# Optimization experiments

Measured on AMD Instinct MI355X. Metric: run time of the kernel, lower is better.

Reference implementation:

```python
import jax, jax.numpy as jnp
import numpy as np

TAU = 0.01  # softmax temperature used throughout the module


def _cross_en(sim_matrix):
    # -mean(diag(log_softmax(sim, -1)))
    logpt = jax.nn.log_softmax(sim_matrix, axis=-1)
    return -jnp.mean(jnp.diagonal(logpt))


def setup_inputs() -> dict:
    key = jax.random.key(0)
    k1, k2, k3, k4 = jax.random.split(key, 4)
    bs, nw, nf, d = 128, 80, 64, 768
    inp = {
        "traj_output": jax.random.normal(k1, (bs, d), dtype=jnp.float32),
        "frame_features": jax.random.normal(k2, (bs, nf, d), dtype=jnp.float32),
        "sentence_output": jax.random.normal(k3, (bs, d), dtype=jnp.float32),
        "word_features": jax.random.normal(k4, (bs, nw, d), dtype=jnp.float32),
        # nn.Parameter(torch.eye(...)) -- init_weights does not touch these
        "global_mat_weight": jnp.eye(d, dtype=jnp.float32),
        "word_logit_weight": jnp.eye(nw, dtype=jnp.float32),
        "frame_logit_weight": jnp.eye(nf, dtype=jnp.float32),
        "local_mat_weight": jnp.eye(d, dtype=jnp.float32),
        "frame_mat_weight": jnp.eye(nf, dtype=jnp.float32),
        "word_mat_weight": jnp.eye(nw, dtype=jnp.float32),
        "frame_mat_weight2": jnp.eye(nf, dtype=jnp.float32),
        "word_mat_weight2": jnp.eye(nw, dtype=jnp.float32),
    }
    return inp


def reference(traj_output, frame_features, sentence_output, word_features,
              global_mat_weight, word_logit_weight, frame_logit_weight,
              local_mat_weight, frame_mat_weight, word_mat_weight,
              frame_mat_weight2, word_mat_weight2):
    # traj_output: [bs,d]; frame_features: [bs,nf,d]; sentence_output: [bs,d]; word_features: [bs,nw,d]

    # --- traj_sent: (sent @ G) @ traj^T -> [bs_t, bs_v] ---
    traj_sent_sim = (sentence_output @ global_mat_weight) @ traj_output.T

    # --- video_word: word_features @ traj^T -> [bs_t, nw, bs_v] ---
    A = jnp.einsum('twd,vd->twv', word_features, traj_output)
    sA = jax.nn.softmax(A / TAU, axis=1)
    # (softmax.permute(0,2,1) @ W).permute(0,2,1): contract nw axis with W
    wA = jnp.einsum('twv,wu->tuv', sA, word_logit_weight)
    video_word_sim = jnp.sum(A * wA, axis=1)  # [bs_t, bs_v]

    # --- sentence_frame: sent x frame -> [bs_v, bs_t, nf] (torch broadcast batching) ---
    B = jnp.einsum('td,vfd->vtf', sentence_output, frame_features)
    sB = jax.nn.softmax(B / TAU, axis=-1)
    sentence_frame_sim = jnp.sum(B * (sB @ frame_logit_weight), axis=-1).T  # [bs_t, bs_v]

    # --- frame_word: fine-grained sim [bs_t, nw, bs_v, nf] ---
    S = jnp.einsum('twd,vfd->twvf', word_features @ local_mat_weight, frame_features)
    # word-level logit: softmax over nw, mix with word_mat_weight, weighted sum over nw
    sw = jax.nn.softmax(S / TAU, axis=1)
    word_level = jnp.sum(jnp.einsum('twvf,wu->tuvf', sw, word_mat_weight) * S, axis=1)  # [t,v,f]
    # frame-level logit: softmax over nf, mix with frame_mat_weight, weighted sum over nf
    sf = jax.nn.softmax(S / TAU, axis=-1)
    frame_level = jnp.sum((sf @ frame_mat_weight) * S, axis=-1)  # [t,w,v]
    # sent2frame: reduce nf of word_level
    smw = jax.nn.softmax(word_level / TAU, axis=-1)
    sent2frame = jnp.sum((smw @ frame_mat_weight2) * word_level, axis=-1)  # [t,v]
    # video2word: reduce nw of frame_level
    smf = jax.nn.softmax(frame_level / TAU, axis=1)
    video2word = jnp.sum(jnp.einsum('twv,wu->tuv', smf, word_mat_weight2) * frame_level, axis=1)  # [t,v]
    frame_word_sim = (sent2frame + video2word) / 2.0

    sim_matrix = (traj_sent_sim + video_word_sim + sentence_frame_sim + frame_word_sim) / 4.0

    sim_loss = (_cross_en(sim_matrix) + _cross_en(sim_matrix.T)) / 2.0
    return sim_loss
```

## Files before the change

kernel.cpp:

```cpp
#include <hip/hip_runtime.h>
#include <math.h>

#define BS 128
#define NW 80
#define NF 64
#define DD 768
#define INV_TAU 100.0f

typedef unsigned short u16;
typedef unsigned int u32;
typedef __attribute__((ext_vector_type(8))) short bf16x8;
typedef __attribute__((ext_vector_type(4))) float f32x4;

__device__ __forceinline__ u16 f2bf(float x) {
    unsigned b = __float_as_uint(x);
    return (u16)((b + 0x7fffu + ((b >> 16) & 1u)) >> 16);
}
__device__ __forceinline__ float bf2f(u16 h) { return __uint_as_float(((unsigned)h) << 16); }

__device__ __forceinline__ void gload_lds16(const void* gsrc, void* ldst) {
    __builtin_amdgcn_global_load_lds(
        (const __attribute__((address_space(1))) unsigned int*)gsrc,
        (__attribute__((address_space(3))) unsigned int*)ldst, 16, 0, 0);
}

__global__ __launch_bounds__(256) void k_sent_global(
    const float* __restrict__ sent, const float* __restrict__ G, float* __restrict__ sg)
{
    int idx = blockIdx.x * 256 + threadIdx.x;
    int t = idx / DD, e = idx % DD;
    const float* srow = sent + t * DD;
    float acc = 0.f;
    #pragma unroll 4
    for (int d = 0; d < DD; ++d) acc += srow[d] * G[d * DD + e];
    sg[idx] = acc;
}

__global__ __launch_bounds__(256) void k_traj_sent(
    const float* __restrict__ sg, const float* __restrict__ traj, float* __restrict__ sim)
{
    __shared__ float ss[16][33], tt[16][33];
    int tx = threadIdx.x & 15, ty = threadIdx.x >> 4;
    int t0 = blockIdx.y * 16, v0 = blockIdx.x * 16;
    float acc = 0.f;
    for (int kk = 0; kk < DD; kk += 32) {
        for (int l = threadIdx.x; l < 16 * 32; l += 256) {
            int r = l >> 5, c = l & 31;
            ss[r][c] = sg[(t0 + r) * DD + kk + c];
            tt[r][c] = traj[(v0 + r) * DD + kk + c];
        }
        __syncthreads();
        #pragma unroll
        for (int k = 0; k < 32; ++k) acc += ss[ty][k] * tt[tx][k];
        __syncthreads();
    }
    sim[(t0 + ty) * BS + v0 + tx] = 0.25f * acc;
}

__global__ __launch_bounds__(256) void k_prepw(
    const float* __restrict__ Wm, const float* __restrict__ Fm,
    u16* __restrict__ WmT_hi, u16* __restrict__ WmT_lo,
    u16* __restrict__ FmT_hi, u16* __restrict__ FmT_lo)
{
    int gid = blockIdx.x * 256 + threadIdx.x;
    if (gid < 80 * 96) {
        int u = gid / 96, w = gid % 96;
        float x = (w < 80) ? Wm[w * 80 + u] : 0.f;
        u16 h = f2bf(x);
        WmT_hi[gid] = h; WmT_lo[gid] = f2bf(x - bf2f(h));
    } else if (gid < 80 * 96 + 64 * 64) {
        int j = gid - 80 * 96;
        int fp = j >> 6, f = j & 63;
        float x = Fm[f * 64 + fp];
        u16 h = f2bf(x);
        FmT_hi[j] = h; FmT_lo[j] = f2bf(x - bf2f(h));
    }
}

__global__ __launch_bounds__(256) void k_ffsplit(
    const float* __restrict__ x, u16* __restrict__ hi, u16* __restrict__ lo)
{
    int i = blockIdx.x * 256 + threadIdx.x;
    float4 f = *(const float4*)&x[(size_t)i * 4];
    ushort4 h, l;
    h.x = f2bf(f.x); l.x = f2bf(f.x - bf2f(h.x));
    h.y = f2bf(f.y); l.y = f2bf(f.y - bf2f(h.y));
    h.z = f2bf(f.z); l.z = f2bf(f.z - bf2f(h.z));
    h.w = f2bf(f.w); l.w = f2bf(f.w - bf2f(h.w));
    *(ushort4*)&hi[(size_t)i * 4] = h;
    *(ushort4*)&lo[(size_t)i * 4] = l;
}

__global__ __launch_bounds__(256, 2) void k_wl(
    const float* __restrict__ wf, const float* __restrict__ L,
    u16* __restrict__ wl_hi, u16* __restrict__ wl_lo)
{
    __shared__ u16 Ah[128][72], Al[128][72];
    __shared__ u16 Bh[128][72], Bl[128][72];
    const int tid = threadIdx.x;
    const int lane = tid & 63, wid = tid >> 6;
    const int m0 = blockIdx.y * 128, n0 = blockIdx.x * 128;

    f32x4 acc[2][8];
    #pragma unroll
    for (int i = 0; i < 2; ++i)
        #pragma unroll
        for (int j = 0; j < 8; ++j) acc[i][j] = (f32x4){0.f, 0.f, 0.f, 0.f};

    for (int kk = 0; kk < DD; kk += 64) {
        #pragma unroll
        for (int p = 0; p < 8; ++p) {
            int row = p * 16 + (tid >> 4), c4 = tid & 15;
            float4 v = *(const float4*)&wf[(size_t)(m0 + row) * DD + kk + c4 * 4];
            ushort4 h, l;
            h.x = f2bf(v.x); l.x = f2bf(v.x - bf2f(h.x));
            h.y = f2bf(v.y); l.y = f2bf(v.y - bf2f(h.y));
            h.z = f2bf(v.z); l.z = f2bf(v.z - bf2f(h.z));
            h.w = f2bf(v.w); l.w = f2bf(v.w - bf2f(h.w));
            *(ushort4*)&Ah[row][c4 * 4] = h;
            *(ushort4*)&Al[row][c4 * 4] = l;
        }
        #pragma unroll
        for (int p = 0; p < 8; ++p) {
            int kr = p * 8 + (tid >> 5), c4 = tid & 31;
            float4 v = *(const float4*)&L[(size_t)(kk + kr) * DD + n0 + c4 * 4];
            #pragma unroll
            for (int jj = 0; jj < 4; ++jj) {
                int n = c4 * 4 + jj;
                float x = (jj == 0) ? v.x : (jj == 1) ? v.y : (jj == 2) ? v.z : v.w;
                u16 h = f2bf(x);
                int ka = kr ^ ((n & 7) << 3);
                Bh[n][ka] = h;
                Bl[n][ka] = f2bf(x - bf2f(h));
            }
        }
        __syncthreads();
        #pragma unroll
        for (int ks = 0; ks < 2; ++ks) {
            int koff = ks * 32 + (lane >> 4) * 8;
            bf16x8 ah[2], al[2];
            #pragma unroll
            for (int i = 0; i < 2; ++i) {
                int row = wid * 32 + 16 * i + (lane & 15);
                ah[i] = *(const bf16x8*)&Ah[row][koff];
                al[i] = *(const bf16x8*)&Al[row][koff];
            }
            #pragma unroll
            for (int j = 0; j < 8; ++j) {
                int n = 16 * j + (lane & 15);
                int kb = koff ^ ((n & 7) << 3);
                bf16x8 bh = *(const bf16x8*)&Bh[n][kb];
                bf16x8 bl = *(const bf16x8*)&Bl[n][kb];
                #pragma unroll
                for (int i = 0; i < 2; ++i) {
                    acc[i][j] = __builtin_amdgcn_mfma_f32_16x16x32_bf16(ah[i], bh, acc[i][j], 0, 0, 0);
                    acc[i][j] = __builtin_amdgcn_mfma_f32_16x16x32_bf16(ah[i], bl, acc[i][j], 0, 0, 0);
                    acc[i][j] = __builtin_amdgcn_mfma_f32_16x16x32_bf16(al[i], bh, acc[i][j], 0, 0, 0);
                }
            }
        }
        __syncthreads();
    }
    #pragma unroll
    for (int i = 0; i < 2; ++i)
        #pragma unroll
        for (int j = 0; j < 8; ++j)
            #pragma unroll
            for (int r = 0; r < 4; ++r) {
                float x = acc[i][j][r];
                int row = m0 + wid * 32 + 16 * i + ((lane >> 4) << 2) + r;
                int col = n0 + 16 * j + (lane & 15);
                size_t idx = (size_t)row * DD + col;
                u16 h = f2bf(x);
                wl_hi[idx] = h;
                wl_lo[idx] = f2bf(x - bf2f(h));
            }
}

__global__ __launch_bounds__(256, 2) void k_video_word(
    const float* __restrict__ wf, const float* __restrict__ traj,
    const float* __restrict__ Wl, float* __restrict__ sim)
{
    __shared__ __align__(16) float As[NW][36];
    __shared__ __align__(16) float Bs[64][36];
    __shared__ float Am[NW][65];
    __shared__ float Pm[NW][65];
    int tx = threadIdx.x & 15, ty = threadIdx.x >> 4;
    int t = blockIdx.y, v0 = blockIdx.x * 64;
    const float* wft = wf + t * NW * DD;
    float acc[5][4] = {};
    for (int kk = 0; kk < DD; kk += 32) {
        for (int l = threadIdx.x; l < NW * 32; l += 256) {
            int w = l >> 5, k = l & 31;
            As[w][k] = wft[w * DD + kk + k];
        }
        for (int l = threadIdx.x; l < 64 * 32; l += 256) {
            int v = l >> 5, k = l & 31;
            Bs[v][k] = traj[(v0 + v) * DD + kk + k];
        }
        __syncthreads();
        #pragma unroll
        for (int k = 0; k < 32; k += 4) {
            float4 a[5], b[4];
            #pragma unroll
            for (int i = 0; i < 5; ++i) a[i] = *(const float4*)&As[tx + 16 * i][k];
            #pragma unroll
            for (int j = 0; j < 4; ++j) b[j] = *(const float4*)&Bs[ty + 16 * j][k];
            #pragma unroll
            for (int i = 0; i < 5; ++i)
                #pragma unroll
                for (int j = 0; j < 4; ++j)
                    acc[i][j] += a[i].x * b[j].x + a[i].y * b[j].y + a[i].z * b[j].z + a[i].w * b[j].w;
        }
        __syncthreads();
    }
    #pragma unroll
    for (int i = 0; i < 5; ++i)
        #pragma unroll
        for (int j = 0; j < 4; ++j) Am[tx + 16 * i][ty + 16 * j] = acc[i][j];
    __syncthreads();
    if (threadIdx.x < 64) {
        int v = threadIdx.x;
        float m = -1e30f;
        for (int w = 0; w < NW; ++w) m = fmaxf(m, Am[w][v]);
        float s = 0.f;
        for (int w = 0; w < NW; ++w) { float e = __expf((Am[w][v] - m) * INV_TAU); Pm[w][v] = e; s += e; }
        float r = 1.f / s;
        for (int w = 0; w < NW; ++w) Pm[w][v] *= r;
    }
    __syncthreads();
    float mm[5][4] = {};
    for (int w = 0; w < NW; ++w) {
        float a[5], b[4];
        #pragma unroll
        for (int i = 0; i < 5; ++i) a[i] = Wl[w * NW + tx + 16 * i];
        #pragma unroll
        for (int j = 0; j < 4; ++j) b[j] = Pm[w][ty + 16 * j];
        #pragma unroll
        for (int i = 0; i < 5; ++i)
            #pragma unroll
            for (int j = 0; j < 4; ++j) mm[i][j] += a[i] * b[j];
    }
    #pragma unroll
    for (int j = 0; j < 4; ++j) {
        float p = 0.f;
        #pragma unroll
        for (int i = 0; i < 5; ++i) p += mm[i][j] * Am[tx + 16 * i][ty + 16 * j];
        for (int o = 8; o; o >>= 1) p += __shfl_xor(p, o, 16);
        if (tx == 0) sim[t * BS + v0 + ty + 16 * j] += 0.25f * p;
    }
}

__global__ __launch_bounds__(256, 2) void k_sent_frame(
    const float* __restrict__ sent, const float* __restrict__ ff,
    const float* __restrict__ Fl, float* __restrict__ sim)
{
    __shared__ __align__(16) float Ss[64][36];
    __shared__ __align__(16) float Fs[64][36];
    __shared__ float Bm[64][65];
    __shared__ float Pm[64][65];
    int tx = threadIdx.x & 15, ty = threadIdx.x >> 4;
    int v = blockIdx.y, t0 = blockIdx.x * 64;
    const float* ffv = ff + v * NF * DD;
    float acc[4][4] = {};
    for (int kk = 0; kk < DD; kk += 32) {
        for (int l = threadIdx.x; l < 64 * 32; l += 256) {
            int r = l >> 5, k = l & 31;
            Ss[r][k] = sent[(t0 + r) * DD + kk + k];
            Fs[r][k] = ffv[r * DD + kk + k];
        }
        __syncthreads();
        #pragma unroll
        for (int k = 0; k < 32; k += 4) {
            float4 a[4], b[4];
            #pragma unroll
            for (int i = 0; i < 4; ++i) a[i] = *(const float4*)&Ss[tx + 16 * i][k];
            #pragma unroll
            for (int j = 0; j < 4; ++j) b[j] = *(const float4*)&Fs[ty + 16 * j][k];
            #pragma unroll
            for (int i = 0; i < 4; ++i)
                #pragma unroll
                for (int j = 0; j < 4; ++j)
                    acc[i][j] += a[i].x * b[j].x + a[i].y * b[j].y + a[i].z * b[j].z + a[i].w * b[j].w;
        }
        __syncthreads();
    }
    #pragma unroll
    for (int i = 0; i < 4; ++i)
        #pragma unroll
        for (int j = 0; j < 4; ++j) Bm[tx + 16 * i][ty + 16 * j] = acc[i][j];
    __syncthreads();
    if (threadIdx.x < 64) {
        int r = threadIdx.x;
        float m = -1e30f;
        for (int f = 0; f < NF; ++f) m = fmaxf(m, Bm[r][f]);
        float s = 0.f;
        for (int f = 0; f < NF; ++f) { float e = __expf((Bm[r][f] - m) * INV_TAU); Pm[r][f] = e; s += e; }
        float rr = 1.f / s;
        for (int f = 0; f < NF; ++f) Pm[r][f] *= rr;
    }
    __syncthreads();
    float nn[4][4] = {};
    for (int f = 0; f < NF; ++f) {
        float a[4], b[4];
        #pragma unroll
        for (int i = 0; i < 4; ++i) a[i] = Pm[ty + 16 * i][f];
        #pragma unroll
        for (int j = 0; j < 4; ++j) b[j] = Fl[f * NF + tx + 16 * j];
        #pragma unroll
        for (int i = 0; i < 4; ++i)
            #pragma unroll
            for (int j = 0; j < 4; ++j) nn[i][j] += a[i] * b[j];
    }
    #pragma unroll
    for (int i = 0; i < 4; ++i) {
        float p = 0.f;
        #pragma unroll
        for (int j = 0; j < 4; ++j) p += nn[i][j] * Bm[ty + 16 * i][tx + 16 * j];
        for (int o = 8; o; o >>= 1) p += __shfl_xor(p, o, 16);
        if (tx == 0) sim[(t0 + ty + 16 * i) * BS + v] += 0.25f * p;
    }
}

__global__ __launch_bounds__(256, 4) void k_frame_word(
    const u16* __restrict__ wl_hi, const u16* __restrict__ wl_lo,
    const u16* __restrict__ ff_hi, const u16* __restrict__ ff_lo,
    const u16* __restrict__ WmT_hi, const u16* __restrict__ WmT_lo,
    const u16* __restrict__ FmT_hi, const u16* __restrict__ FmT_lo,
    const float* __restrict__ F2, const float* __restrict__ Wm2,
    float* __restrict__ sim)
{
    __shared__ __align__(16) union SH {
        u16 stage[18432];
        struct Post {
            float Sm[80][65];
            float redm[4][64], reds[4][64];
            float colM[64], colRD[64];
            float rowM[80], rowRD[80];
            float wlv[64], flv[80], flvp[4][80];
            float smw[64], smf[80];
            float s2f, v2w;
        } post;
    } sh;

    const int tid = threadIdx.x;
    const int lane = tid & 63, wid = tid >> 6;
    const int col = lane & 15, grp = lane >> 4;
    const int v = blockIdx.x, t = blockIdx.y;

    f32x4 acc[5], acc2[5];
    #pragma unroll
    for (int i = 0; i < 5; ++i) { acc[i] = (f32x4){0.f,0.f,0.f,0.f}; acc2[i] = (f32x4){0.f,0.f,0.f,0.f}; }

    const int r8 = lane >> 3, s8 = lane & 7;
    const int gk = s8 ^ r8;

    for (int kk = 0; kk < DD; kk += 64) {
        for (int seg = wid; seg < 36; seg += 4) {
            const u16* src;
            int ldsoff;
            if (seg < 10) {
                int g = seg, row = g * 8 + r8;
                src = wl_hi + (size_t)(t * NW + row) * DD + kk + gk * 8;
                ldsoff = g * 512;
            } else if (seg < 20) {
                int g = seg - 10, row = g * 8 + r8;
                src = wl_lo + (size_t)(t * NW + row) * DD + kk + gk * 8;
                ldsoff = 5120 + g * 512;
            } else if (seg < 28) {
                int g = seg - 20, row = g * 8 + r8;
                src = ff_hi + (size_t)(v * NF + row) * DD + kk + gk * 8;
                ldsoff = 10240 + g * 512;
            } else {
                int g = seg - 28, row = g * 8 + r8;
                src = ff_lo + (size_t)(v * NF + row) * DD + kk + gk * 8;
                ldsoff = 14336 + g * 512;
            }
            gload_lds16(src, (void*)&sh.stage[ldsoff]);
        }
        __syncthreads();
        const u16* st = sh.stage;
        #pragma unroll
        for (int ks = 0; ks < 2; ++ks) {
            const int sl = (ks << 2) + grp;
            bf16x8 afh[5], afl[5], bfh, bfl;
            #pragma unroll
            for (int i = 0; i < 5; ++i) {
                int row = col + 16 * i;
                int off = row * 64 + ((sl ^ (row & 7)) << 3);
                afh[i] = *(const bf16x8*)&st[off];
                afl[i] = *(const bf16x8*)&st[5120 + off];
            }
            {
                int row = col + 16 * wid;
                int off = row * 64 + ((sl ^ (row & 7)) << 3);
                bfh = *(const bf16x8*)&st[10240 + off];
                bfl = *(const bf16x8*)&st[14336 + off];
            }
            #pragma unroll
            for (int i = 0; i < 5; ++i)
                acc[i] = __builtin_amdgcn_mfma_f32_16x16x32_bf16(afh[i], bfh, acc[i], 0, 0, 0);
            #pragma unroll
            for (int i = 0; i < 5; ++i)
                acc2[i] = __builtin_amdgcn_mfma_f32_16x16x32_bf16(afh[i], bfl, acc2[i], 0, 0, 0);
            #pragma unroll
            for (int i = 0; i < 5; ++i)
                acc[i] = __builtin_amdgcn_mfma_f32_16x16x32_bf16(afl[i], bfh, acc[i], 0, 0, 0);
        }
        __syncthreads();
    }

    #pragma unroll
    for (int i = 0; i < 5; ++i)
        #pragma unroll
        for (int r = 0; r < 4; ++r)
            sh.post.Sm[16 * i + (grp << 2) + r][col + (wid << 4)] = acc[i][r] + acc2[i][r];
    __syncthreads();

    {
        const int f = tid & 63, q = tid >> 6, w0 = q * 20;
        float m = -1e30f;
        for (int w = w0; w < w0 + 20; ++w) m = fmaxf(m, sh.post.Sm[w][f]);
        float s = 0.f;
        for (int w = w0; w < w0 + 20; ++w) s += __expf((sh.post.Sm[w][f] - m) * INV_TAU);
        sh.post.redm[q][f] = m; sh.post.reds[q][f] = s;
        __syncthreads();
        if (q == 0) {
            float M = -1e30f;
            #pragma unroll
            for (int qq = 0; qq < 4; ++qq) M = fmaxf(M, sh.post.redm[qq][f]);
            float Dn = 0.f;
            #pragma unroll
            for (int qq = 0; qq < 4; ++qq) Dn += sh.post.reds[qq][f] * __expf((sh.post.redm[qq][f] - M) * INV_TAU);
            sh.post.colM[f] = M;
            sh.post.colRD[f] = 1.f / Dn;
        }
    }
    __syncthreads();

    {
        f32x4 d1[5], d1b[5];
        #pragma unroll
        for (int i = 0; i < 5; ++i) { d1[i] = (f32x4){0.f,0.f,0.f,0.f}; d1b[i] = (f32x4){0.f,0.f,0.f,0.f}; }
        const int f = wid * 16 + col;
        const float Mf = sh.post.colM[f], RDf = sh.post.colRD[f];
        #pragma unroll
        for (int ks = 0; ks < 3; ++ks) {
            const int w0 = ks * 32 + grp * 8;
            union { u16 h[8]; bf16x8 v; } bh, bl;
            #pragma unroll
            for (int j = 0; j < 8; ++j) {
                int w = w0 + j;
                int wc = (w < NW) ? w : 0;
                float e = __expf((sh.post.Sm[wc][f] - Mf) * INV_TAU) * RDf;
                e = (w < NW) ? e : 0.f;
                u16 hh = f2bf(e);
                bh.h[j] = hh;
                bl.h[j] = f2bf(e - bf2f(hh));
            }
            #pragma unroll
            for (int i = 0; i < 5; ++i) {
                int aaddr = (16 * i + col) * 96 + ks * 32 + grp * 8;
                bf16x8 ah = *(const bf16x8*)&WmT_hi[aaddr];
                bf16x8 al = *(const bf16x8*)&WmT_lo[aaddr];
                d1[i]  = __builtin_amdgcn_mfma_f32_16x16x32_bf16(ah, bh.v, d1[i], 0, 0, 0);
                d1b[i] = __builtin_amdgcn_mfma_f32_16x16x32_bf16(ah, bl.v, d1b[i], 0, 0, 0);
                d1[i]  = __builtin_amdgcn_mfma_f32_16x16x32_bf16(al, bh.v, d1[i], 0, 0, 0);
            }
        }
        float p = 0.f;
        #pragma unroll
        for (int i = 0; i < 5; ++i)
            #pragma unroll
            for (int r = 0; r < 4; ++r)
                p += (d1[i][r] + d1b[i][r]) * sh.post.Sm[16 * i + (grp << 2) + r][f];
        p += __shfl_xor(p, 16);
        p += __shfl_xor(p, 32);
        if (lane < 16) sh.post.wlv[wid * 16 + lane] = p;
    }
    __syncthreads();

    if (tid < 160) {
        const int w = tid >> 1, h = tid & 1, f0 = h * 32;
        float m = -1e30f;
        for (int c = 0; c < 32; ++c) m = fmaxf(m, sh.post.Sm[w][f0 + c]);
        m = fmaxf(m, __shfl_xor(m, 1));
        float s = 0.f;
        for (int c = 0; c < 32; ++c) s += __expf((sh.post.Sm[w][f0 + c] - m) * INV_TAU);
        s += __shfl_xor(s, 1);
        if (h == 0) { sh.post.rowM[w] = m; sh.post.rowRD[w] = 1.f / s; }
    }
    __syncthreads();

    {
        f32x4 d2[5], d2b[5];
        #pragma unroll
        for (int i = 0; i < 5; ++i) { d2[i] = (f32x4){0.f,0.f,0.f,0.f}; d2b[i] = (f32x4){0.f,0.f,0.f,0.f}; }
        #pragma unroll
        for (int ks = 0; ks < 2; ++ks) {
            int baddr = (wid * 16 + col) * 64 + ks * 32 + grp * 8;
            bf16x8 bh = *(const bf16x8*)&FmT_hi[baddr];
            bf16x8 bl = *(const bf16x8*)&FmT_lo[baddr];
            #pragma unroll
            for (int i = 0; i < 5; ++i) {
                const int row = 16 * i + col;
                const float Mw = sh.post.rowM[row], RDw = sh.post.rowRD[row];
                const int f0 = ks * 32 + grp * 8;
                union { u16 h[8]; bf16x8 v; } ah, al;
                #pragma unroll
                for (int j = 0; j < 8; ++j) {
                    float e = __expf((sh.post.Sm[row][f0 + j] - Mw) * INV_TAU) * RDw;
                    u16 hh = f2bf(e);
                    ah.h[j] = hh;
                    al.h[j] = f2bf(e - bf2f(hh));
                }
                d2[i]  = __builtin_amdgcn_mfma_f32_16x16x32_bf16(ah.v, bh, d2[i], 0, 0, 0);
                d2b[i] = __builtin_amdgcn_mfma_f32_16x16x32_bf16(ah.v, bl, d2b[i], 0, 0, 0);
                d2[i]  = __builtin_amdgcn_mfma_f32_16x16x32_bf16(al.v, bh, d2[i], 0, 0, 0);
            }
        }
        #pragma unroll
        for (int i = 0; i < 5; ++i)
            #pragma unroll
            for (int r = 0; r < 4; ++r) {
                int w = 16 * i + (grp << 2) + r;
                float p = (d2[i][r] + d2b[i][r]) * sh.post.Sm[w][wid * 16 + col];
                p += __shfl_xor(p, 1);
                p += __shfl_xor(p, 2);
                p += __shfl_xor(p, 4);
                p += __shfl_xor(p, 8);
                if (col == 0) sh.post.flvp[wid][w] = p;
            }
    }
    __syncthreads();
    if (tid < 80)
        sh.post.flv[tid] = sh.post.flvp[0][tid] + sh.post.flvp[1][tid]
                         + sh.post.flvp[2][tid] + sh.post.flvp[3][tid];
    __syncthreads();

    if (wid == 0) {
        float x = sh.post.wlv[lane];
        float m = x;
        #pragma unroll
        for (int o = 32; o; o >>= 1) m = fmaxf(m, __shfl_xor(m, o));
        float e = __expf((x - m) * INV_TAU);
        float s = e;
        #pragma unroll
        for (int o = 32; o; o >>= 1) s += __shfl_xor(s, o);
        sh.post.smw[lane] = e / s;
    } else if (wid == 1) {
        float x0 = sh.post.flv[lane];
        float x1 = (lane < 16) ? sh.post.flv[64 + lane] : -1e30f;
        float m = fmaxf(x0, x1);
        #pragma unroll
        for (int o = 32; o; o >>= 1) m = fmaxf(m, __shfl_xor(m, o));
        float e0 = __expf((x0 - m) * INV_TAU);
        float e1 = (lane < 16) ? __expf((x1 - m) * INV_TAU) : 0.f;
        float s = e0 + e1;
        #pragma unroll
        for (int o = 32; o; o >>= 1) s += __shfl_xor(s, o);
        sh.post.smf[lane] = e0 / s;
        if (lane < 16) sh.post.smf[64 + lane] = e1 / s;
    }
    __syncthreads();

    if (wid == 0) {
        float g = 0.f;
        for (int f = 0; f < NF; ++f) g += sh.post.smw[f] * F2[f * NF + lane];
        float p = g * sh.post.wlv[lane];
        #pragma unroll
        for (int o = 32; o; o >>= 1) p += __shfl_xor(p, o);
        if (lane == 0) sh.post.s2f = p;
    } else if (wid == 1) {
        float g = 0.f;
        for (int w = 0; w < NW; ++w) g += sh.post.smf[w] * Wm2[w * NW + lane];
        float p = g * sh.post.flv[lane];
        if (lane < 16) {
            float g2 = 0.f;
            for (int w = 0; w < NW; ++w) g2 += sh.post.smf[w] * Wm2[w * NW + 64 + lane];
            p += g2 * sh.post.flv[64 + lane];
        }
        #pragma unroll
        for (int o = 32; o; o >>= 1) p += __shfl_xor(p, o);
        if (lane == 0) sh.post.v2w = p;
    }
    __syncthreads();
    if (tid == 0) sim[t * BS + v] += 0.125f * (sh.post.s2f + sh.post.v2w);
}

__global__ __launch_bounds__(256) void k_loss(const float* __restrict__ sim, float* __restrict__ out)
{
    __shared__ float S[BS][BS + 1];
    __shared__ float lr[BS], lc[BS];
    for (int l = threadIdx.x; l < BS * BS; l += 256) {
        int r = l >> 7, c = l & 127;
        S[r][c] = sim[l];
    }
    __syncthreads();
    int tid = threadIdx.x;
    if (tid < BS) {
        float m = -1e30f;
        for (int c = 0; c < BS; ++c) m = fmaxf(m, S[tid][c]);
        float s = 0.f;
        for (int c = 0; c < BS; ++c) s += __expf(S[tid][c] - m);
        lr[tid] = m + __logf(s);
    } else {
        int c = tid - BS;
        float m = -1e30f;
        for (int r = 0; r < BS; ++r) m = fmaxf(m, S[r][c]);
        float s = 0.f;
        for (int r = 0; r < BS; ++r) s += __expf(S[r][c] - m);
        lc[c] = m + __logf(s);
    }
    __syncthreads();
    if (tid == 0) {
        float a = 0.f;
        for (int i = 0; i < BS; ++i) a += S[i][i] - 0.5f * lr[i] - 0.5f * lc[i];
        out[0] = -a / (float)BS;
    }
}

extern "C" void kernel_launch(void* const* d_in, const int* in_sizes, int n_in,
                              void* d_out, int out_size, void* d_ws, size_t ws_size,
                              hipStream_t stream)
{
    const float* traj = (const float*)d_in[0];
    const float* ff   = (const float*)d_in[1];
    const float* sent = (const float*)d_in[2];
    const float* wf   = (const float*)d_in[3];
    const float* G    = (const float*)d_in[4];
    const float* Wl   = (const float*)d_in[5];
    const float* Fl   = (const float*)d_in[6];
    const float* L    = (const float*)d_in[7];
    const float* Fm   = (const float*)d_in[8];
    const float* Wm   = (const float*)d_in[9];
    const float* F2   = (const float*)d_in[10];
    const float* Wm2  = (const float*)d_in[11];
    float* out = (float*)d_out;
    char* base = (char*)d_ws;

    float* sg     = (float*)(base);
    float* sim    = (float*)(base + 393216);
    u16*   wl_hi  = (u16*)(base + 458752);
    u16*   wl_lo  = (u16*)(base + 16187392);
    u16*   ff_hi  = (u16*)(base + 31916032);
    u16*   ff_lo  = (u16*)(base + 44498944);
    u16*   WmT_hi = (u16*)(base + 57081856);
    u16*   WmT_lo = (u16*)(base + 57097216);
    u16*   FmT_hi = (u16*)(base + 57112576);
    u16*   FmT_lo = (u16*)(base + 57120768);

    hipLaunchKernelGGL(k_sent_global, dim3(BS * DD / 256), dim3(256), 0, stream, sent, G, sg);
    hipLaunchKernelGGL(k_traj_sent, dim3(8, 8), dim3(256), 0, stream, sg, traj, sim);
    hipLaunchKernelGGL(k_prepw, dim3(46), dim3(256), 0, stream, Wm, Fm, WmT_hi, WmT_lo, FmT_hi, FmT_lo);
    hipLaunchKernelGGL(k_ffsplit, dim3(BS * NF * DD / 1024), dim3(256), 0, stream, ff, ff_hi, ff_lo);
    hipLaunchKernelGGL(k_wl, dim3(6, 80), dim3(256), 0, stream, wf, L, wl_hi, wl_lo);
    hipLaunchKernelGGL(k_video_word, dim3(2, BS), dim3(256), 0, stream, wf, traj, Wl, sim);
    hipLaunchKernelGGL(k_sent_frame, dim3(2, BS), dim3(256), 0, stream, sent, ff, Fl, sim);
    hipLaunchKernelGGL(k_frame_word, dim3(BS, BS), dim3(256), 0, stream,
                       wl_hi, wl_lo, ff_hi, ff_lo, WmT_hi, WmT_lo, FmT_hi, FmT_lo, F2, Wm2, sim);
    hipLaunchKernelGGL(k_loss, dim3(1), dim3(256), 0, stream, sim, out);
}
```

Measured before the change: 1.483 ms.

## Restructure frame-word epilogue: apply softmax after weight mixing, keep S in registers

The post-GEMM stage of k_frame_word no longer stores S as fp32 in shared memory and exponentiates it inside the MFMA operand build. It splits S once into bf16 hi/lo copies in two layouts and multiplies S by the mixing weights with MFMA. The softmax probabilities are computed in registers with shuffle reductions and applied afterwards, relying on linearity so normalisation becomes a scalar multiply. This cuts repeated exp evaluations, shared-memory traffic and some barriers. In exchange the weight prep layout changes, launch bounds drop to 3 blocks per SIMD, and the bf16 split of S changes the rounding error profile.

After: 1.905 ms. 28.4% more time.

```diff
diff --git a/kernel.cpp b/kernel.cpp
--- a/kernel.cpp
+++ b/kernel.cpp
@@ -59,21 +59,20 @@
 
 __global__ __launch_bounds__(256) void k_prepw(
     const float* __restrict__ Wm, const float* __restrict__ Fm,
-    u16* __restrict__ WmT_hi, u16* __restrict__ WmT_lo,
-    u16* __restrict__ FmT_hi, u16* __restrict__ FmT_lo)
+    u16* __restrict__ Wm_hi, u16* __restrict__ Wm_lo,
+    u16* __restrict__ Fm_hi, u16* __restrict__ Fm_lo)
 {
     int gid = blockIdx.x * 256 + threadIdx.x;
     if (gid < 80 * 96) {
-        int u = gid / 96, w = gid % 96;
-        float x = (w < 80) ? Wm[w * 80 + u] : 0.f;
+        int w = gid / 96, u = gid % 96;
+        float x = (u < 80) ? Wm[w * 80 + u] : 0.f;
         u16 h = f2bf(x);
-        WmT_hi[gid] = h; WmT_lo[gid] = f2bf(x - bf2f(h));
+        Wm_hi[gid] = h; Wm_lo[gid] = f2bf(x - bf2f(h));
     } else if (gid < 80 * 96 + 64 * 64) {
         int j = gid - 80 * 96;
-        int fp = j >> 6, f = j & 63;
-        float x = Fm[f * 64 + fp];
+        float x = Fm[j];
         u16 h = f2bf(x);
-        FmT_hi[j] = h; FmT_lo[j] = f2bf(x - bf2f(h));
+        Fm_hi[j] = h; Fm_lo[j] = f2bf(x - bf2f(h));
     }
 }
 
@@ -322,22 +321,22 @@
     }
 }
 
-__global__ __launch_bounds__(256, 4) void k_frame_word(
+__global__ __launch_bounds__(256, 3) void k_frame_word(
     const u16* __restrict__ wl_hi, const u16* __restrict__ wl_lo,
     const u16* __restrict__ ff_hi, const u16* __restrict__ ff_lo,
-    const u16* __restrict__ WmT_hi, const u16* __restrict__ WmT_lo,
-    const u16* __restrict__ FmT_hi, const u16* __restrict__ FmT_lo,
+    const u16* __restrict__ Wm_hi, const u16* __restrict__ Wm_lo,
+    const u16* __restrict__ Fm_hi, const u16* __restrict__ Fm_lo,
     const float* __restrict__ F2, const float* __restrict__ Wm2,
     float* __restrict__ sim)
 {
     __shared__ __align__(16) union SH {
         u16 stage[18432];
         struct Post {
-            float Sm[80][65];
-            float redm[4][64], reds[4][64];
-            float colM[64], colRD[64];
+            u16 Swf_h[80][72], Swf_l[80][72];
+            u16 Sfw_h[64][104], Sfw_l[64][104];
+            float part[2][4][80];
             float rowM[80], rowRD[80];
-            float wlv[64], flv[80], flvp[4][80];
+            float wlv[64], flv[80];
             float smw[64], smf[80];
             float s2f, v2w;
         } post;
@@ -347,6 +346,7 @@
     const int lane = tid & 63, wid = tid >> 6;
     const int col = lane & 15, grp = lane >> 4;
     const int v = blockIdx.x, t = blockIdx.y;
+    const int myf = col + 16 * wid;
 
     f32x4 acc[5], acc2[5];
     #pragma unroll
@@ -410,132 +410,167 @@
         __syncthreads();
     }
 
+    float sv[5][4];
     #pragma unroll
     for (int i = 0; i < 5; ++i)
         #pragma unroll
-        for (int r = 0; r < 4; ++r)
-            sh.post.Sm[16 * i + (grp << 2) + r][col + (wid << 4)] = acc[i][r] + acc2[i][r];
-    __syncthreads();
+        for (int r = 0; r < 4; ++r) sv[i][r] = acc[i][r] + acc2[i][r];
 
     {
-        const int f = tid & 63, q = tid >> 6, w0 = q * 20;
-        float m = -1e30f;
-        for (int w = w0; w < w0 + 20; ++w) m = fmaxf(m, sh.post.Sm[w][f]);
-        float s = 0.f;
-        for (int w = w0; w < w0 + 20; ++w) s += __expf((sh.post.Sm[w][f] - m) * INV_TAU);
-        sh.post.redm[q][f] = m; sh.post.reds[q][f] = s;
-        __syncthreads();
-        if (q == 0) {
-            float M = -1e30f;
-            #pragma unroll
-            for (int qq = 0; qq < 4; ++qq) M = fmaxf(M, sh.post.redm[qq][f]);
-            float Dn = 0.f;
-            #pragma unroll
-            for (int qq = 0; qq < 4; ++qq) Dn += sh.post.reds[qq][f] * __expf((sh.post.redm[qq][f] - M) * INV_TAU);
-            sh.post.colM[f] = M;
-            sh.post.colRD[f] = 1.f / Dn;
-        }
-    }
-    __syncthreads();
-
+        int fz = tid >> 2, qz = tid & 3;
+        ushort4 z = {0, 0, 0, 0};
+        *(ushort4*)&sh.post.Sfw_h[fz][80 + 4 * qz] = z;
+        *(ushort4*)&sh.post.Sfw_l[fz][80 + 4 * qz] = z;
+    }
+    #pragma unroll
+    for (int i = 0; i < 5; ++i) {
+        ushort4 hv, lv;
+        #pragma unroll
+        for (int r = 0; r < 4; ++r) {
+            float x = sv[i][r];
+            u16 h = f2bf(x), l = f2bf(x - bf2f(h));
+            if (r == 0) { hv.x = h; lv.x = l; } else if (r == 1) { hv.y = h; lv.y = l; }
+            else if (r == 2) { hv.z = h; lv.z = l; } else { hv.w = h; lv.w = l; }
+            sh.post.Swf_h[16 * i + 4 * grp + r][myf] = h;
+            sh.post.Swf_l[16 * i + 4 * grp + r][myf] = l;
+        }
+        *(ushort4*)&sh.post.Sfw_h[myf][16 * i + 4 * grp] = hv;
+        *(ushort4*)&sh.post.Sfw_l[myf][16 * i + 4 * grp] = lv;
+    }
+    #pragma unroll
+    for (int i = 0; i < 5; ++i)
+        #pragma unroll
+        for (int r = 0; r < 4; ++r) {
+            float m = sv[i][r];
+            m = fmaxf(m, __shfl_xor(m, 1)); m = fmaxf(m, __shfl_xor(m, 2));
+            m = fmaxf(m, __shfl_xor(m, 4)); m = fmaxf(m, __shfl_xor(m, 8));
+            if (col == 0) sh.post.part[0][wid][16 * i + 4 * grp + r] = m;
+        }
+
+    float cm = -1e30f;
+    #pragma unroll
+    for (int i = 0; i < 5; ++i)
+        #pragma unroll
+        for (int r = 0; r < 4; ++r) cm = fmaxf(cm, sv[i][r]);
+    cm = fmaxf(cm, __shfl_xor(cm, 16));
+    cm = fmaxf(cm, __shfl_xor(cm, 32));
+    float p1[5][4], cs = 0.f;
+    #pragma unroll
+    for (int i = 0; i < 5; ++i)
+        #pragma unroll
+        for (int r = 0; r < 4; ++r) { p1[i][r] = __expf((sv[i][r] - cm) * INV_TAU); cs += p1[i][r]; }
+    cs += __shfl_xor(cs, 16);
+    cs += __shfl_xor(cs, 32);
+    const float cRD = 1.f / cs;
+
+    __syncthreads();
+
+    if (tid < 80) {
+        float m = sh.post.part[0][0][tid];
+        m = fmaxf(m, sh.post.part[0][1][tid]);
+        m = fmaxf(m, sh.post.part[0][2][tid]);
+        m = fmaxf(m, sh.post.part[0][3][tid]);
+        sh.post.rowM[tid] = m;
+    }
+
+    f32x4 e1[5], e2[5];
+    #pragma unroll
+    for (int i = 0; i < 5; ++i) { e1[i] = (f32x4){0.f,0.f,0.f,0.f}; e2[i] = (f32x4){0.f,0.f,0.f,0.f}; }
+    #pragma unroll
+    for (int ks = 0; ks < 3; ++ks) {
+        const int ko = ks * 32 + grp * 8;
+        bf16x8 bh = *(const bf16x8*)&sh.post.Sfw_h[myf][ko];
+        bf16x8 bl = *(const bf16x8*)&sh.post.Sfw_l[myf][ko];
+        bf16x8 ah[5], al[5];
+        #pragma unroll
+        for (int i = 0; i < 5; ++i) {
+            int aaddr = (col + 16 * i) * 96 + ko;
+            ah[i] = *(const bf16x8*)&Wm_hi[aaddr];
+            al[i] = *(const bf16x8*)&Wm_lo[aaddr];
+        }
+        #pragma unroll
+        for (int i = 0; i < 5; ++i)
+            e1[i] = __builtin_amdgcn_mfma_f32_16x16x32_bf16(ah[i], bh, e1[i], 0, 0, 0);
+        #pragma unroll
+        for (int i = 0; i < 5; ++i)
+            e2[i] = __builtin_amdgcn_mfma_f32_16x16x32_bf16(ah[i], bl, e2[i], 0, 0, 0);
+        #pragma unroll
+        for (int i = 0; i < 5; ++i)
+            e1[i] = __builtin_amdgcn_mfma_f32_16x16x32_bf16(al[i], bh, e1[i], 0, 0, 0);
+    }
     {
-        f32x4 d1[5], d1b[5];
-        #pragma unroll
-        for (int i = 0; i < 5; ++i) { d1[i] = (f32x4){0.f,0.f,0.f,0.f}; d1b[i] = (f32x4){0.f,0.f,0.f,0.f}; }
-        const int f = wid * 16 + col;
-        const float Mf = sh.post.colM[f], RDf = sh.post.colRD[f];
-        #pragma unroll
-        for (int ks = 0; ks < 3; ++ks) {
-            const int w0 = ks * 32 + grp * 8;
-            union { u16 h[8]; bf16x8 v; } bh, bl;
-            #pragma unroll
-            for (int j = 0; j < 8; ++j) {
-                int w = w0 + j;
-                int wc = (w < NW) ? w : 0;
-                float e = __expf((sh.post.Sm[wc][f] - Mf) * INV_TAU) * RDf;
-                e = (w < NW) ? e : 0.f;
-                u16 hh = f2bf(e);
-                bh.h[j] = hh;
-                bl.h[j] = f2bf(e - bf2f(hh));
-            }
-            #pragma unroll
-            for (int i = 0; i < 5; ++i) {
-                int aaddr = (16 * i + col) * 96 + ks * 32 + grp * 8;
-                bf16x8 ah = *(const bf16x8*)&WmT_hi[aaddr];
-                bf16x8 al = *(const bf16x8*)&WmT_lo[aaddr];
-                d1[i]  = __builtin_amdgcn_mfma_f32_16x16x32_bf16(ah, bh.v, d1[i], 0, 0, 0);
-                d1b[i] = __builtin_amdgcn_mfma_f32_16x16x32_bf16(ah, bl.v, d1b[i], 0, 0, 0);
-                d1[i]  = __builtin_amdgcn_mfma_f32_16x16x32_bf16(al, bh.v, d1[i], 0, 0, 0);
-            }
-        }
         float p = 0.f;
         #pragma unroll
         for (int i = 0; i < 5; ++i)
             #pragma unroll
-            for (int r = 0; r < 4; ++r)
-                p += (d1[i][r] + d1b[i][r]) * sh.post.Sm[16 * i + (grp << 2) + r][f];
+            for (int r = 0; r < 4; ++r) p += p1[i][r] * (e1[i][r] + e2[i][r]);
         p += __shfl_xor(p, 16);
         p += __shfl_xor(p, 32);
-        if (lane < 16) sh.post.wlv[wid * 16 + lane] = p;
-    }
-    __syncthreads();
-
-    if (tid < 160) {
-        const int w = tid >> 1, h = tid & 1, f0 = h * 32;
-        float m = -1e30f;
-        for (int c = 0; c < 32; ++c) m = fmaxf(m, sh.post.Sm[w][f0 + c]);
-        m = fmaxf(m, __shfl_xor(m, 1));
-        float s = 0.f;
-        for (int c = 0; c < 32; ++c) s += __expf((sh.post.Sm[w][f0 + c] - m) * INV_TAU);
-        s += __shfl_xor(s, 1);
-        if (h == 0) { sh.post.rowM[w] = m; sh.post.rowRD[w] = 1.f / s; }
-    }
-    __syncthreads();
-
-    {
-        f32x4 d2[5], d2b[5];
-        #pragma unroll
-        for (int i = 0; i < 5; ++i) { d2[i] = (f32x4){0.f,0.f,0.f,0.f}; d2b[i] = (f32x4){0.f,0.f,0.f,0.f}; }
-        #pragma unroll
-        for (int ks = 0; ks < 2; ++ks) {
-            int baddr = (wid * 16 + col) * 64 + ks * 32 + grp * 8;
-            bf16x8 bh = *(const bf16x8*)&FmT_hi[baddr];
-            bf16x8 bl = *(const bf16x8*)&FmT_lo[baddr];
-            #pragma unroll
-            for (int i = 0; i < 5; ++i) {
-                const int row = 16 * i + col;
-                const float Mw = sh.post.rowM[row], RDw = sh.post.rowRD[row];
-                const int f0 = ks * 32 + grp * 8;
-                union { u16 h[8]; bf16x8 v; } ah, al;
-                #pragma unroll
-                for (int j = 0; j < 8; ++j) {
-                    float e = __expf((sh.post.Sm[row][f0 + j] - Mw) * INV_TAU) * RDw;
-                    u16 hh = f2bf(e);
-                    ah.h[j] = hh;
-                    al.h[j] = f2bf(e - bf2f(hh));
-                }
-                d2[i]  = __builtin_amdgcn_mfma_f32_16x16x32_bf16(ah.v, bh, d2[i], 0, 0, 0);
-                d2b[i] = __builtin_amdgcn_mfma_f32_16x16x32_bf16(ah.v, bl, d2b[i], 0, 0, 0);
-                d2[i]  = __builtin_amdgcn_mfma_f32_16x16x32_bf16(al.v, bh, d2[i], 0, 0, 0);
-            }
-        }
-        #pragma unroll
-        for (int i = 0; i < 5; ++i)
-            #pragma unroll
-            for (int r = 0; r < 4; ++r) {
-                int w = 16 * i + (grp << 2) + r;
-                float p = (d2[i][r] + d2b[i][r]) * sh.post.Sm[w][wid * 16 + col];
-                p += __shfl_xor(p, 1);
-                p += __shfl_xor(p, 2);
-                p += __shfl_xor(p, 4);
-                p += __shfl_xor(p, 8);
-                if (col == 0) sh.post.flvp[wid][w] = p;
-            }
-    }
-    __syncthreads();
+        if (lane < 16) sh.post.wlv[myf] = p * cRD;
+    }
+
+    __syncthreads();
+
+    float p2[5][4];
+    #pragma unroll
+    for (int i = 0; i < 5; ++i)
+        #pragma unroll
+        for (int r = 0; r < 4; ++r) {
+            float Mw = sh.post.rowM[16 * i + 4 * grp + r];
+            p2[i][r] = __expf((sv[i][r] - Mw) * INV_TAU);
+            float s = p2[i][r];
+            s += __shfl_xor(s, 1); s += __shfl_xor(s, 2);
+            s += __shfl_xor(s, 4); s += __shfl_xor(s, 8);
+            if (col == 0) sh.post.part[1][wid][16 * i + 4 * grp + r] = s;
+        }
+
+    __syncthreads();
+
     if (tid < 80)
-        sh.post.flv[tid] = sh.post.flvp[0][tid] + sh.post.flvp[1][tid]
-                         + sh.post.flvp[2][tid] + sh.post.flvp[3][tid];
+        sh.post.rowRD[tid] = 1.f / (sh.post.part[1][0][tid] + sh.post.part[1][1][tid]
+                                  + sh.post.part[1][2][tid] + sh.post.part[1][3][tid]);
+
+    f32x4 g1[5], g2[5];
+    #pragma unroll
+    for (int i = 0; i < 5; ++i) { g1[i] = (f32x4){0.f,0.f,0.f,0.f}; g2[i] = (f32x4){0.f,0.f,0.f,0.f}; }
+    #pragma unroll
+    for (int ks = 0; ks < 2; ++ks) {
+        const int ko = ks * 32 + grp * 8;
+        bf16x8 bh = *(const bf16x8*)&Fm_hi[myf * 64 + ko];
+        bf16x8 bl = *(const bf16x8*)&Fm_lo[myf * 64 + ko];
+        bf16x8 ah[5], al[5];
+        #pragma unroll
+        for (int i = 0; i < 5; ++i) {
+            int aaddr = (col + 16 * i) * 72 + ko;
+            ah[i] = *(const bf16x8*)&sh.post.Swf_h[0][aaddr];
+            al[i] = *(const bf16x8*)&sh.post.Swf_l[0][aaddr];
+        }
+        #pragma unroll
+        for (int i = 0; i < 5; ++i)
+            g1[i] = __builtin_amdgcn_mfma_f32_16x16x32_bf16(ah[i], bh, g1[i], 0, 0, 0);
+        #pragma unroll
+        for (int i = 0; i < 5; ++i)
+            g2[i] = __builtin_amdgcn_mfma_f32_16x16x32_bf16(ah[i], bl, g2[i], 0, 0, 0);
+        #pragma unroll
+        for (int i = 0; i < 5; ++i)
+            g1[i] = __builtin_amdgcn_mfma_f32_16x16x32_bf16(al[i], bh, g1[i], 0, 0, 0);
+    }
+    #pragma unroll
+    for (int i = 0; i < 5; ++i)
+        #pragma unroll
+        for (int r = 0; r < 4; ++r) {
+            float p = p2[i][r] * (g1[i][r] + g2[i][r]);
+            p += __shfl_xor(p, 1); p += __shfl_xor(p, 2);
+            p += __shfl_xor(p, 4); p += __shfl_xor(p, 8);
+            if (col == 0) sh.post.part[0][wid][16 * i + 4 * grp + r] = p;
+        }
+
+    __syncthreads();
+
+    if (tid < 80)
+        sh.post.flv[tid] = sh.post.rowRD[tid] * (sh.post.part[0][0][tid] + sh.post.part[0][1][tid]
+                                               + sh.post.part[0][2][tid] + sh.post.part[0][3][tid]);
+
     __syncthreads();
 
     if (wid == 0) {
@@ -645,19 +680,19 @@
     u16*   wl_lo  = (u16*)(base + 16187392);
     u16*   ff_hi  = (u16*)(base + 31916032);
     u16*   ff_lo  = (u16*)(base + 44498944);
-    u16*   WmT_hi = (u16*)(base + 57081856);
-    u16*   WmT_lo = (u16*)(base + 57097216);
-    u16*   FmT_hi = (u16*)(base + 57112576);
-    u16*   FmT_lo = (u16*)(base + 57120768);
+    u16*   Wm_hi  = (u16*)(base + 57081856);
+    u16*   Wm_lo  = (u16*)(base + 57097216);
+    u16*   Fm_hi  = (u16*)(base + 57112576);
+    u16*   Fm_lo  = (u16*)(base + 57120768);
 
     hipLaunchKernelGGL(k_sent_global, dim3(BS * DD / 256), dim3(256), 0, stream, sent, G, sg);
     hipLaunchKernelGGL(k_traj_sent, dim3(8, 8), dim3(256), 0, stream, sg, traj, sim);
-    hipLaunchKernelGGL(k_prepw, dim3(46), dim3(256), 0, stream, Wm, Fm, WmT_hi, WmT_lo, FmT_hi, FmT_lo);
+    hipLaunchKernelGGL(k_prepw, dim3(46), dim3(256), 0, stream, Wm, Fm, Wm_hi, Wm_lo, Fm_hi, Fm_lo);
     hipLaunchKernelGGL(k_ffsplit, dim3(BS * NF * DD / 1024), dim3(256), 0, stream, ff, ff_hi, ff_lo);
     hipLaunchKernelGGL(k_wl, dim3(6, 80), dim3(256), 0, stream, wf, L, wl_hi, wl_lo);
     hipLaunchKernelGGL(k_video_word, dim3(2, BS), dim3(256), 0, stream, wf, traj, Wl, sim);
     hipLaunchKernelGGL(k_sent_frame, dim3(2, BS), dim3(256), 0, stream, sent, ff, Fl, sim);
     hipLaunchKernelGGL(k_frame_word, dim3(BS, BS), dim3(256), 0, stream,
-                       wl_hi, wl_lo, ff_hi, ff_lo, WmT_hi, WmT_lo, FmT_hi, FmT_lo, F2, Wm2, sim);
+                       wl_hi, wl_lo, ff_hi, ff_lo, Wm_hi, Wm_lo, Fm_hi, Fm_lo, F2, Wm2, sim);
     hipLaunchKernelGGL(k_loss, dim3(1), dim3(256), 0, stream, sim, out);
 }
```
